# Kernel tuning notes

Measured on AMD Instinct MI355X. Metric: run time of the kernel, lower is better.

## Reference

```python
import jax, jax.numpy as jnp
import numpy as np

TAU = 0.07          # temperature
NUM_CLASSES = 1000  # label vocabulary size (used for bincount length)


def setup_inputs() -> dict:
    key = jax.random.key(0)
    kq, kk, ky = jax.random.split(key, 3)
    N, K, D = 8192, 8, 512
    q = jax.random.normal(kq, (N, D), dtype=jnp.float32)
    q = q / jnp.linalg.norm(q, axis=1, keepdims=True)          # L2-normalized anchors
    k = jax.random.normal(kk, (N, K, D), dtype=jnp.float32)
    k = k / jnp.linalg.norm(k, axis=2, keepdims=True)          # L2-normalized positives
    y = jax.random.randint(ky, (N,), 0, NUM_CLASSES, dtype=jnp.int32)
    return {"q": q, "k": k, "y": y}


def reference(q, k, y):
    # q: [N, D] anchors, k: [N, K, D] external positives, y: [N] labels
    N, K, D = k.shape
    neg_inf = jnp.float32(-jnp.inf)

    # similarities to external positives and within-batch, scaled by temperature
    k_sims = jnp.einsum('nd,nkd->nk', q, k) / TAU            # [N, K]
    batch_sims = jnp.matmul(q, q.T) / TAU                    # [N, N]

    same = y[:, None] == y[None, :]                          # [N, N] label equality
    eye = jnp.eye(N, dtype=bool)
    same_class_mask = same & ~eye                            # in-batch positives (excl. self)
    same_class_counts = same_class_mask.sum(axis=1) + K      # [N]

    # faithful to torch: multiply by mask then masked_fill(x == 0, -inf)
    batch_pos = batch_sims * same_class_mask
    batch_pos = jnp.where(batch_pos == 0, neg_inf, batch_pos)
    pos_sims = jnp.concatenate([k_sims, batch_pos], axis=1)  # [N, K+N]
    num = jax.scipy.special.logsumexp(pos_sims, axis=1)      # [N]

    y_counts = jnp.bincount(y, length=NUM_CLASSES)           # [C]
    neg_sims = batch_sims * (~same)
    neg_sims = jnp.where(neg_sims == 0, neg_inf, neg_sims)
    # class-frequency-weighted denominator (as in the original, no max-shift)
    den = jnp.log(jnp.sum(jnp.exp(neg_sims) / y_counts[y][None, :].astype(q.dtype), axis=1))

    loss = -(num - den) / same_class_counts.astype(q.dtype)
    return loss.mean()
```

## Files before the change

### kernel.cpp

```cpp
#include <hip/hip_runtime.h>
#include <stdint.h>

constexpr int N    = 8192;
constexpr int D    = 512;
constexpr int KEXT = 8;
constexpr int NCLS = 1000;
#define TAU_INV  14.285714285714285714f
#define SQRT_TI  3.7796447300922722f

constexpr int BM = 128, BN = 128;
constexpr int NB   = N / BM;
constexpr int NBLK = NB * (NB + 1) / 2;

typedef _Float16 half8 __attribute__((ext_vector_type(8)));
typedef float    f32x4 __attribute__((ext_vector_type(4)));

__global__ void prep_k(const float* __restrict__ q, const int* __restrict__ y,
                       _Float16* __restrict__ qf, int* __restrict__ counts,
                       float* __restrict__ invc, float* __restrict__ pos,
                       float* __restrict__ neg) {
    const int b = blockIdx.x, tid = threadIdx.x;
    if (b == 0) {
        __shared__ int h[NCLS];
        for (int i = tid; i < NCLS; i += 256) h[i] = 0;
        __syncthreads();
        for (int i = tid; i < N; i += 256) atomicAdd(&h[y[i]], 1);
        __syncthreads();
        for (int i = tid; i < NCLS; i += 256) {
            int c = h[i];
            counts[i] = c;
            invc[i]   = 1.0f / (float)c;
        }
        return;
    }
    const int gid = (b - 1) * 256 + tid;
    const int row = gid >> 6;
    const int cg  = gid & 63;
    const float4* src = reinterpret_cast<const float4*>(q + (size_t)row * D + cg * 8);
    float4 v0 = src[0], v1 = src[1];
    half8 o;
    o[0] = (_Float16)(v0.x * SQRT_TI); o[1] = (_Float16)(v0.y * SQRT_TI);
    o[2] = (_Float16)(v0.z * SQRT_TI); o[3] = (_Float16)(v0.w * SQRT_TI);
    o[4] = (_Float16)(v1.x * SQRT_TI); o[5] = (_Float16)(v1.y * SQRT_TI);
    o[6] = (_Float16)(v1.z * SQRT_TI); o[7] = (_Float16)(v1.w * SQRT_TI);
    const int t = row >> 4, l15 = row & 15, ks = cg >> 2, quad = cg & 3;
    reinterpret_cast<half8*>(qf)[(size_t)(t * 16 + ks) * 64 + quad * 16 + l15] = o;
    if (gid < N) { pos[gid] = 0.f; neg[gid] = 0.f; }
}

__global__ __launch_bounds__(256, 2) void gemm_k(
        const _Float16* __restrict__ qf,
        const int* __restrict__ y,
        const float* __restrict__ invc,
        float* __restrict__ pos_sum,
        float* __restrict__ neg_sum) {
    __shared__ int   yis[BM];
    __shared__ int   yjs[BN];
    __shared__ float icsA[BM];
    __shared__ float icsB[BN];

    const int tid  = threadIdx.x;
    const int wave = tid >> 6;
    const int lane = tid & 63;
    const int quad = lane >> 4;
    const int l15  = lane & 15;

    const int t0 = blockIdx.x;
    const int t  = (t0 & 7) * (NBLK / 8) + (t0 >> 3);

    int bi = (int)(((float)(2 * NB + 1) -
                    sqrtf((float)((2 * NB + 1) * (2 * NB + 1)) - 8.0f * (float)t)) * 0.5f);
    if (bi < 0) bi = 0;
    if (bi > NB - 1) bi = NB - 1;
    while ((bi + 1) * NB - ((bi + 1) * bi >> 1) <= t) ++bi;
    while (bi * NB - (bi * (bi - 1) >> 1) > t) --bi;
    const int bj = bi + (t - (bi * NB - (bi * (bi - 1) >> 1)));
    const int ibase = bi * BM, jbase = bj * BN;

    if (tid < BM) {
        int yi = y[ibase + tid];
        int yj = y[jbase + tid];
        yis[tid] = yi;  icsA[tid] = invc[yi];
        yjs[tid] = yj;  icsB[tid] = invc[yj];
    }
    __syncthreads();

    const int wr = (wave >> 1) * 64;
    const int wc = (wave & 1) * 64;

    f32x4 acc[4][4];
#pragma unroll
    for (int a = 0; a < 4; a++)
#pragma unroll
        for (int b = 0; b < 4; b++) acc[a][b] = (f32x4)0.0f;

    const half8* fb = reinterpret_cast<const half8*>(qf);
    const half8* pA[4];
    const half8* pB[4];
#pragma unroll
    for (int m = 0; m < 4; m++) {
        pA[m] = fb + (size_t)((bi * 8) + (wr >> 4) + m) * 1024 + lane;
        pB[m] = fb + (size_t)((bj * 8) + (wc >> 4) + m) * 1024 + lane;
    }

    half8 af[2][4], bf[2][4];
#pragma unroll
    for (int m = 0; m < 4; m++) { af[0][m] = pA[m][0]; bf[0][m] = pB[m][0]; }

#pragma unroll
    for (int ks = 0; ks < 16; ks++) {
        const int cur = ks & 1, nxt = cur ^ 1;
        if (ks < 15) {
#pragma unroll
            for (int m = 0; m < 4; m++) {
                af[nxt][m] = pA[m][(ks + 1) * 64];
                bf[nxt][m] = pB[m][(ks + 1) * 64];
            }
        }
#pragma unroll
        for (int mi = 0; mi < 4; mi++)
#pragma unroll
            for (int mj = 0; mj < 4; mj++)
                acc[mi][mj] = __builtin_amdgcn_mfma_f32_16x16x32_f16(af[cur][mi], bf[cur][mj], acc[mi][mj], 0, 0, 0);
    }

    int   yjv[4];
    float icj[4];
#pragma unroll
    for (int mj = 0; mj < 4; mj++) {
        int jl = wc + mj * 16 + l15;
        yjv[mj] = yjs[jl];
        icj[mj] = icsB[jl];
    }

    if (bi == bj) {
#pragma unroll
        for (int mi = 0; mi < 4; mi++) {
#pragma unroll
            for (int r = 0; r < 4; r++) {
                const int il   = wr + mi * 16 + quad * 4 + r;
                const int irow = ibase + il;
                const int yi   = yis[il];
                float posp = 0.f, negp = 0.f;
#pragma unroll
                for (int mj = 0; mj < 4; mj++) {
                    const int jcol = jbase + wc + mj * 16 + l15;
                    float a    = acc[mi][mj][r];
                    float e    = __expf(a);
                    bool  nz   = (a != 0.0f);
                    bool  same = (yi == yjv[mj]);
                    posp += (same && (irow != jcol) && nz) ? e : 0.0f;
                    negp += (!same && nz) ? e * icj[mj] : 0.0f;
                }
#pragma unroll
                for (int off = 1; off < 16; off <<= 1) {
                    posp += __shfl_xor(posp, off);
                    negp += __shfl_xor(negp, off);
                }
                if (l15 == 0) {
                    atomicAdd(&pos_sum[irow], posp);
                    atomicAdd(&neg_sum[irow], negp);
                }
            }
        }
    } else {
        float cp[4] = {0.f, 0.f, 0.f, 0.f};
        float cn[4] = {0.f, 0.f, 0.f, 0.f};
#pragma unroll
        for (int mi = 0; mi < 4; mi++) {
#pragma unroll
            for (int r = 0; r < 4; r++) {
                const int il   = wr + mi * 16 + quad * 4 + r;
                const int irow = ibase + il;
                const int yi   = yis[il];
                const float ici = icsA[il];
                float posp = 0.f, negp = 0.f;
#pragma unroll
                for (int mj = 0; mj < 4; mj++) {
                    float a    = acc[mi][mj][r];
                    float e    = __expf(a);
                    bool  nz   = (a != 0.0f);
                    bool  same = (yi == yjv[mj]);
                    float pe   = (same && nz) ? e : 0.0f;
                    posp   += pe;
                    cp[mj] += pe;
                    negp   += (!same && nz) ? e * icj[mj] : 0.0f;
                    cn[mj] += (!same && nz) ? e * ici : 0.0f;
                }
#pragma unroll
                for (int off = 1; off < 16; off <<= 1) {
                    posp += __shfl_xor(posp, off);
                    negp += __shfl_xor(negp, off);
                }
                if (l15 == 0) {
                    atomicAdd(&pos_sum[irow], posp);
                    atomicAdd(&neg_sum[irow], negp);
                }
            }
        }
#pragma unroll
        for (int mj = 0; mj < 4; mj++) {
            float a = cp[mj], b = cn[mj];
            a += __shfl_xor(a, 16); a += __shfl_xor(a, 32);
            b += __shfl_xor(b, 16); b += __shfl_xor(b, 32);
            if (quad == 0) {
                const int jcol = jbase + wc + mj * 16 + l15;
                atomicAdd(&pos_sum[jcol], a);
                atomicAdd(&neg_sum[jcol], b);
            }
        }
    }
}

__global__ void finalize_k(const float* __restrict__ q, const float* __restrict__ kmat,
                           const int* __restrict__ y, const int* __restrict__ counts,
                           const float* __restrict__ pos_sum, const float* __restrict__ neg_sum,
                           float* __restrict__ loss) {
    const int wave = threadIdx.x >> 6, lane = threadIdx.x & 63;
    const int i = blockIdx.x * 4 + wave;

    const float4* q4 = reinterpret_cast<const float4*>(q) + (size_t)i * 128;
    const float4* k4 = reinterpret_cast<const float4*>(kmat) + (size_t)i * KEXT * 128;
    float4 qa = q4[lane], qb = q4[lane + 64];

    float esum = 0.f;
    for (int kk = 0; kk < KEXT; kk++) {
        float4 ka = k4[(size_t)kk * 128 + lane];
        float4 kb = k4[(size_t)kk * 128 + lane + 64];
        float p = qa.x * ka.x;
        p = fmaf(qa.y, ka.y, p); p = fmaf(qa.z, ka.z, p); p = fmaf(qa.w, ka.w, p);
        p = fmaf(qb.x, kb.x, p); p = fmaf(qb.y, kb.y, p);
        p = fmaf(qb.z, kb.z, p); p = fmaf(qb.w, kb.w, p);
#pragma unroll
        for (int off = 1; off < 64; off <<= 1) p += __shfl_xor(p, off);
        esum += __expf(p * TAU_INV);
    }
    if (lane == 0) {
        float num = logf(esum + pos_sum[i]);
        float den = logf(neg_sum[i]);
        float cnt = (float)(counts[y[i]] - 1 + KEXT);
        loss[i] = -(num - den) / cnt;
    }
}

__global__ void reduce_k(const float* __restrict__ loss, float* __restrict__ out) {
    __shared__ float part[16];
    int tid = threadIdx.x;
    float s = 0.f;
    for (int i = tid; i < N; i += 1024) s += loss[i];
#pragma unroll
    for (int off = 1; off < 64; off <<= 1) s += __shfl_xor(s, off);
    if ((tid & 63) == 0) part[tid >> 6] = s;
    __syncthreads();
    if (tid < 16) {
        float v = part[tid];
#pragma unroll
        for (int off = 1; off < 16; off <<= 1) v += __shfl_xor(v, off);
        if (tid == 0) out[0] = v / (float)N;
    }
}

extern "C" void kernel_launch(void* const* d_in, const int* in_sizes, int n_in,
                              void* d_out, int out_size, void* d_ws, size_t ws_size,
                              hipStream_t stream) {
    const float* q    = (const float*)d_in[0];
    const float* kmat = (const float*)d_in[1];
    const int*   y    = (const int*)d_in[2];
    float* out = (float*)d_out;

    char* ws = (char*)d_ws;
    _Float16* qf   = (_Float16*)ws;
    int*   counts  = (int*)  (ws + 8388608);
    float* invc    = (float*)(ws + 8392704);
    float* pos     = (float*)(ws + 8396800);
    float* neg     = (float*)(ws + 8429568);
    float* loss    = (float*)(ws + 8462336);

    prep_k    <<<1 + (N * 64) / 256, 256, 0, stream>>>(q, y, qf, counts, invc, pos, neg);
    gemm_k    <<<NBLK, 256, 0, stream>>>(qf, y, invc, pos, neg);
    finalize_k<<<N / 4, 256, 0, stream>>>(q, kmat, y, counts, pos, neg, loss);
    reduce_k  <<<1, 1024, 0, stream>>>(loss, out);
}
```

Measured before the change: 360.4 us.

## Switch similarity GEMM from FP16 to FP8 e4m3 MFMA

Quantizes the scaled anchors to FP8 e4m3 in the prep kernel, using a new packed fragment layout, and runs the Gram matrix on fp8 MFMA instructions. This halves operand bytes and uses the higher-throughput fp8 matrix path. It also raises the launch-bounds occupancy hint to 3 and drops the block-index swizzle. The cost is much lower precision in the similarities before exponentiation, which may perturb the loss noticeably. The loss of swizzling may also hurt cache locality.

```diff
diff --git a/kernel.cpp b/kernel.cpp
--- a/kernel.cpp
+++ b/kernel.cpp
@@ -1,4 +1,5 @@
 #include <hip/hip_runtime.h>
+#include <hip/hip_fp8.h>
 #include <stdint.h>
 
 constexpr int N    = 8192;
@@ -12,11 +13,17 @@
 constexpr int NB   = N / BM;
 constexpr int NBLK = NB * (NB + 1) / 2;
 
-typedef _Float16 half8 __attribute__((ext_vector_type(8)));
-typedef float    f32x4 __attribute__((ext_vector_type(4)));
+typedef long   long2_t __attribute__((ext_vector_type(2)));
+typedef float  f32x4   __attribute__((ext_vector_type(4)));
+
+__device__ __forceinline__ uint32_t pack4_e4m3(float a, float b, float c, float d) {
+    __hip_fp8_e4m3 A(a), B(b), C(c), D(d);
+    return (uint32_t)A.__x | ((uint32_t)B.__x << 8) |
+           ((uint32_t)C.__x << 16) | ((uint32_t)D.__x << 24);
+}
 
 __global__ void prep_k(const float* __restrict__ q, const int* __restrict__ y,
-                       _Float16* __restrict__ qf, int* __restrict__ counts,
+                       uint32_t* __restrict__ qf8, int* __restrict__ counts,
                        float* __restrict__ invc, float* __restrict__ pos,
                        float* __restrict__ neg) {
     const int b = blockIdx.x, tid = threadIdx.x;
@@ -34,22 +41,26 @@
         return;
     }
     const int gid = (b - 1) * 256 + tid;
-    const int row = gid >> 6;
-    const int cg  = gid & 63;
-    const float4* src = reinterpret_cast<const float4*>(q + (size_t)row * D + cg * 8);
-    float4 v0 = src[0], v1 = src[1];
-    half8 o;
-    o[0] = (_Float16)(v0.x * SQRT_TI); o[1] = (_Float16)(v0.y * SQRT_TI);
-    o[2] = (_Float16)(v0.z * SQRT_TI); o[3] = (_Float16)(v0.w * SQRT_TI);
-    o[4] = (_Float16)(v1.x * SQRT_TI); o[5] = (_Float16)(v1.y * SQRT_TI);
-    o[6] = (_Float16)(v1.z * SQRT_TI); o[7] = (_Float16)(v1.w * SQRT_TI);
-    const int t = row >> 4, l15 = row & 15, ks = cg >> 2, quad = cg & 3;
-    reinterpret_cast<half8*>(qf)[(size_t)(t * 16 + ks) * 64 + quad * 16 + l15] = o;
+    const int row = gid >> 5;
+    const int c   = gid & 31;
+    const int ks2 = c >> 2, quad = c & 3;
+    const float* src = q + (size_t)row * D + ks2 * 64 + quad * 8;
+    float4 v0 = *reinterpret_cast<const float4*>(src);
+    float4 v1 = *reinterpret_cast<const float4*>(src + 4);
+    float4 v2 = *reinterpret_cast<const float4*>(src + 32);
+    float4 v3 = *reinterpret_cast<const float4*>(src + 36);
+    uint4 o;
+    o.x = pack4_e4m3(v0.x * SQRT_TI, v0.y * SQRT_TI, v0.z * SQRT_TI, v0.w * SQRT_TI);
+    o.y = pack4_e4m3(v1.x * SQRT_TI, v1.y * SQRT_TI, v1.z * SQRT_TI, v1.w * SQRT_TI);
+    o.z = pack4_e4m3(v2.x * SQRT_TI, v2.y * SQRT_TI, v2.z * SQRT_TI, v2.w * SQRT_TI);
+    o.w = pack4_e4m3(v3.x * SQRT_TI, v3.y * SQRT_TI, v3.z * SQRT_TI, v3.w * SQRT_TI);
+    const int t = row >> 4, l15 = row & 15;
+    reinterpret_cast<uint4*>(qf8)[(size_t)t * 512 + ks2 * 64 + quad * 16 + l15] = o;
     if (gid < N) { pos[gid] = 0.f; neg[gid] = 0.f; }
 }
 
-__global__ __launch_bounds__(256, 2) void gemm_k(
-        const _Float16* __restrict__ qf,
+__global__ __launch_bounds__(256, 3) void gemm_k(
+        const uint32_t* __restrict__ qf8,
         const int* __restrict__ y,
         const float* __restrict__ invc,
         float* __restrict__ pos_sum,
@@ -65,9 +76,7 @@
     const int quad = lane >> 4;
     const int l15  = lane & 15;
 
-    const int t0 = blockIdx.x;
-    const int t  = (t0 & 7) * (NBLK / 8) + (t0 >> 3);
-
+    const int t = blockIdx.x;
     int bi = (int)(((float)(2 * NB + 1) -
                     sqrtf((float)((2 * NB + 1) * (2 * NB + 1)) - 8.0f * (float)t)) * 0.5f);
     if (bi < 0) bi = 0;
@@ -94,34 +103,41 @@
 #pragma unroll
         for (int b = 0; b < 4; b++) acc[a][b] = (f32x4)0.0f;
 
-    const half8* fb = reinterpret_cast<const half8*>(qf);
-    const half8* pA[4];
-    const half8* pB[4];
+    const long2_t* fb = reinterpret_cast<const long2_t*>(qf8);
+    const long2_t* pA[4];
+    const long2_t* pB[4];
 #pragma unroll
     for (int m = 0; m < 4; m++) {
-        pA[m] = fb + (size_t)((bi * 8) + (wr >> 4) + m) * 1024 + lane;
-        pB[m] = fb + (size_t)((bj * 8) + (wc >> 4) + m) * 1024 + lane;
-    }
-
-    half8 af[2][4], bf[2][4];
+        pA[m] = fb + (size_t)(bi * 8 + (wr >> 4) + m) * 512 + lane;
+        pB[m] = fb + (size_t)(bj * 8 + (wc >> 4) + m) * 512 + lane;
+    }
+
+    long2_t af[2][4], bf[2][4];
 #pragma unroll
     for (int m = 0; m < 4; m++) { af[0][m] = pA[m][0]; bf[0][m] = pB[m][0]; }
 
 #pragma unroll
-    for (int ks = 0; ks < 16; ks++) {
-        const int cur = ks & 1, nxt = cur ^ 1;
-        if (ks < 15) {
+    for (int ks2 = 0; ks2 < 8; ks2++) {
+        const int cur = ks2 & 1, nxt = cur ^ 1;
+        if (ks2 < 7) {
 #pragma unroll
             for (int m = 0; m < 4; m++) {
-                af[nxt][m] = pA[m][(ks + 1) * 64];
-                bf[nxt][m] = pB[m][(ks + 1) * 64];
+                af[nxt][m] = pA[m][(ks2 + 1) * 64];
+                bf[nxt][m] = pB[m][(ks2 + 1) * 64];
             }
         }
 #pragma unroll
         for (int mi = 0; mi < 4; mi++)
 #pragma unroll
             for (int mj = 0; mj < 4; mj++)
-                acc[mi][mj] = __builtin_amdgcn_mfma_f32_16x16x32_f16(af[cur][mi], bf[cur][mj], acc[mi][mj], 0, 0, 0);
+                acc[mi][mj] = __builtin_amdgcn_mfma_f32_16x16x32_fp8_fp8(
+                    af[cur][mi].x, bf[cur][mj].x, acc[mi][mj], 0, 0, 0);
+#pragma unroll
+        for (int mi = 0; mi < 4; mi++)
+#pragma unroll
+            for (int mj = 0; mj < 4; mj++)
+                acc[mi][mj] = __builtin_amdgcn_mfma_f32_16x16x32_fp8_fp8(
+                    af[cur][mi].y, bf[cur][mj].y, acc[mi][mj], 0, 0, 0);
     }
 
     int   yjv[4];
@@ -269,15 +285,15 @@
     float* out = (float*)d_out;
 
     char* ws = (char*)d_ws;
-    _Float16* qf   = (_Float16*)ws;
-    int*   counts  = (int*)  (ws + 8388608);
-    float* invc    = (float*)(ws + 8392704);
-    float* pos     = (float*)(ws + 8396800);
-    float* neg     = (float*)(ws + 8429568);
-    float* loss    = (float*)(ws + 8462336);
-
-    prep_k    <<<1 + (N * 64) / 256, 256, 0, stream>>>(q, y, qf, counts, invc, pos, neg);
-    gemm_k    <<<NBLK, 256, 0, stream>>>(qf, y, invc, pos, neg);
+    uint32_t* qf8  = (uint32_t*)ws;
+    int*   counts  = (int*)  (ws + 4194304);
+    float* invc    = (float*)(ws + 4198400);
+    float* pos     = (float*)(ws + 4202496);
+    float* neg     = (float*)(ws + 4235264);
+    float* loss    = (float*)(ws + 4268032);
+
+    prep_k    <<<1 + (N * 32) / 256, 256, 0, stream>>>(q, y, qf8, counts, invc, pos, neg);
+    gemm_k    <<<NBLK, 256, 0, stream>>>(qf8, y, invc, pos, neg);
     finalize_k<<<N / 4, 256, 0, stream>>>(q, kmat, y, counts, pos, neg, loss);
     reduce_k  <<<1, 1024, 0, stream>>>(loss, out);
 }
```

Result: no change. 354.2 us (-1.7%).
